# Kernel tuning notes

Hardware: AMD Instinct MI355X
Metric: run time of the kernel (lower is better)

The kernel has to match this reference:

```python
import jax, jax.numpy as jnp
import numpy as np

N = 1024
N_FEAT = 512
HID = 256
N_KERNEL = 10
KERNEL_DIM = 10
MB_DIM = N_KERNEL * KERNEL_DIM  # 100
CAT = HID + N_KERNEL  # concat width per block
EPS = 1e-3  # keras LayerNormalization default epsilon
ALPHA = 0.3  # keras LeakyReLU default


def setup_inputs() -> dict:
    key = jax.random.key(0)
    ks = jax.random.split(key, 16)
    def w(k, shape, std=0.1):
        return (jax.random.normal(k, shape, dtype=jnp.float32) * std)
    return {
        "x": jax.random.normal(ks[0], (N, N_FEAT), dtype=jnp.float32),
        # block 0
        "W0": w(ks[1], (N_FEAT, HID)), "b0": jnp.zeros((HID,), jnp.float32),
        "Wd0": w(ks[2], (HID, MB_DIM)), "bd0": jnp.zeros((MB_DIM,), jnp.float32),
        "beta0": jnp.zeros((CAT,), jnp.float32),
        # block 1 (input width = HID + N_KERNEL)
        "W1": w(ks[3], (CAT, HID)), "b1": jnp.zeros((HID,), jnp.float32),
        "Wd1": w(ks[4], (HID, MB_DIM)), "bd1": jnp.zeros((MB_DIM,), jnp.float32),
        "beta1": jnp.zeros((CAT,), jnp.float32),
        # final critic head
        "Wf": w(ks[5], (CAT, 1)), "bf": jnp.zeros((1,), jnp.float32),
    }


def _batch_diversity(M):
    # M: [N, n_kernel*kernel_dim] -> [N, n_kernel]
    M = M.reshape(-1, N_KERNEL, KERNEL_DIM)
    # pairwise L1 distance over kernel_dim: [N, N, n_kernel]
    l1 = jnp.abs(M[:, None, :, :] - M[None, :, :, :]).sum(axis=3)
    return jnp.exp(-l1).sum(axis=0)  # [N, n_kernel]


def _layer_norm_center_only(h, beta):
    mu = h.mean(axis=-1, keepdims=True)
    var = h.var(axis=-1, keepdims=True)
    return (h - mu) * jax.lax.rsqrt(var + EPS) + beta


def _block(x, W, b, Wd, bd, beta):
    h = x @ W + b                       # [N, HID]
    div = _batch_diversity(h @ Wd + bd)  # [N, N_KERNEL]
    h = jnp.concatenate([h, div], axis=1)  # [N, CAT]
    h = _layer_norm_center_only(h, beta)   # dropout is identity at inference
    return jax.nn.leaky_relu(h, ALPHA)


def reference(x, W0, b0, Wd0, bd0, beta0, W1, b1, Wd1, bd1, beta1, Wf, bf):
    h = _block(x, W0, b0, Wd0, bd0, beta0)
    h = _block(h, W1, b1, Wd1, bd1, beta1)
    return h @ Wf + bf  # [N, 1] critic value (WGGP: no sigmoid)
```

## Files before the change

### kernel.cpp

```cpp
#include <hip/hip_runtime.h>

typedef __attribute__((ext_vector_type(8))) short short8;
typedef __attribute__((ext_vector_type(4))) float f32x4;

#define EPS   1e-3f
#define ALPHA 0.3f

#define MFMA(a, b, c) __builtin_amdgcn_mfma_f32_16x16x32_bf16((a), (b), (c), 0, 0, 0)

__device__ __forceinline__ unsigned short f2bf(float f) {
    unsigned u = __float_as_uint(f);
    unsigned r = u + 0x7FFFu + ((u >> 16) & 1u);
    return (unsigned short)(r >> 16);
}
__device__ __forceinline__ float lrelu(float v) { return v > 0.f ? v : ALPHA * v; }

__global__ __launch_bounds__(256) void prep_kernel(
    const float* __restrict__ W0, const float* __restrict__ Wd0,
    const float* __restrict__ W1, const float* __restrict__ Wd1,
    const float* __restrict__ b0, const float* __restrict__ bd0,
    const float* __restrict__ b1, const float* __restrict__ bd1,
    unsigned short* __restrict__ Wc0bT, unsigned short* __restrict__ Wc1bT,
    float* __restrict__ bcomb0, float* __restrict__ bcomb1)
{
    const int bid = blockIdx.x, t = threadIdx.x;
    if (bid < 100) {
        __shared__ unsigned short Ab[32][264];
        __shared__ unsigned short BbT[32][264];
        const float *Wsrc, *Wdsrc;
        unsigned short* Cdst;
        int ldc, ft, ct, arows;
        if (bid < 64) { ft = bid & 15; ct = bid >> 4; Wsrc = W0; Wdsrc = Wd0;
                        Cdst = Wc0bT; ldc = 512; arows = 512; }
        else { const int s = bid - 64; ft = s % 9; ct = s / 9;
               Wsrc = W1; Wdsrc = Wd1; Cdst = Wc1bT; ldc = 296; arows = 266; }

        {
            const int row = t >> 3, kc = t & 7;
            const int f = ft * 32 + row;
            if (f < arows) {
                const float* wp = Wsrc + (size_t)f * 256 + kc * 32;
#pragma unroll
                for (int i = 0; i < 8; ++i) {
                    const float4 v = ((const float4*)wp)[i];
                    Ab[row][kc * 32 + i * 4 + 0] = f2bf(v.x);
                    Ab[row][kc * 32 + i * 4 + 1] = f2bf(v.y);
                    Ab[row][kc * 32 + i * 4 + 2] = f2bf(v.z);
                    Ab[row][kc * 32 + i * 4 + 3] = f2bf(v.w);
                }
            } else {
#pragma unroll
                for (int i = 0; i < 8; ++i)
                    *(ushort4*)&Ab[row][kc * 32 + i * 4] = make_ushort4(0, 0, 0, 0);
            }
        }
        for (int idx = t; idx < 2048; idx += 256) {
            const int h = idx >> 3, c4 = idx & 7;
            const int cbase = ct * 32 + c4 * 4;
            float v[4];
            if (cbase + 3 < 100) {
                const float4 q = *(const float4*)&Wdsrc[(size_t)h * 100 + cbase];
                v[0] = q.x; v[1] = q.y; v[2] = q.z; v[3] = q.w;
            } else {
#pragma unroll
                for (int j = 0; j < 4; ++j)
                    v[j] = (cbase + j < 100) ? Wdsrc[(size_t)h * 100 + cbase + j] : 0.f;
            }
#pragma unroll
            for (int j = 0; j < 4; ++j) BbT[c4 * 4 + j][h] = f2bf(v[j]);
        }
        __syncthreads();

        const int lane = t & 63, w = t >> 6;
        const int cr = w & 1, fr = w >> 1, r = lane & 15, g = lane >> 4;
        const unsigned short* Ap = &BbT[cr * 16 + r][g * 8];
        const unsigned short* Bp = &Ab[fr * 16 + r][g * 8];
        f32x4 a0 = {0.f, 0.f, 0.f, 0.f}, a1 = {0.f, 0.f, 0.f, 0.f};
#pragma unroll
        for (int k0 = 0; k0 < 256; k0 += 64) {
            a0 = MFMA(*(const short8*)(Ap + k0),      *(const short8*)(Bp + k0),      a0);
            a1 = MFMA(*(const short8*)(Ap + k0 + 32), *(const short8*)(Bp + k0 + 32), a1);
        }
        const f32x4 acc = a0 + a1;
        const int crow = ct * 32 + cr * 16 + g * 4;
        const int fcol = ft * 32 + fr * 16 + r;
#pragma unroll
        for (int i = 0; i < 4; ++i)
            Cdst[(size_t)(crow + i) * ldc + fcol] = f2bf(acc[i]);
    } else {
        const float* bb = (bid == 100) ? b0 : b1;
        const float* Wd = (bid == 100) ? Wd0 : Wd1;
        const float* bd = (bid == 100) ? bd0 : bd1;
        float* o = (bid == 100) ? bcomb0 : bcomb1;
        if (t < 128) {
            float s = 0.f;
            if (t < 100) {
                s = bd[t];
                float s0 = 0.f, s1 = 0.f, s2 = 0.f, s3 = 0.f;
                for (int k = 0; k < 256; k += 4) {
                    s0 += bb[k]     * Wd[k * 100 + t];
                    s1 += bb[k + 1] * Wd[(k + 1) * 100 + t];
                    s2 += bb[k + 2] * Wd[(k + 2) * 100 + t];
                    s3 += bb[k + 3] * Wd[(k + 3) * 100 + t];
                }
                s += (s0 + s1) + (s2 + s3);
            }
            o[t] = s;
        }
    }
}

__global__ __launch_bounds__(256) void hm0_mfma(
    const float* __restrict__ x, const float* __restrict__ W0,
    const unsigned short* __restrict__ Wc0bT,
    const float* __restrict__ b0, const float* __restrict__ bcomb0,
    float* __restrict__ h0, float* __restrict__ Mt0)
{
    __shared__ unsigned short At[32][520];
    __shared__ unsigned short Bt[32][520];

    const int t = threadIdx.x, xt = blockIdx.x, yt = blockIdx.y;

    {
        const int row = t >> 3, kc = t & 7;
        const float* xp = x + (size_t)(xt * 32 + row) * 512 + kc * 64;
#pragma unroll
        for (int i = 0; i < 8; ++i) {
            const float4 lo = ((const float4*)xp)[i * 2];
            const float4 hi = ((const float4*)xp)[i * 2 + 1];
            short8 p;
            p[0] = f2bf(lo.x); p[1] = f2bf(lo.y); p[2] = f2bf(lo.z); p[3] = f2bf(lo.w);
            p[4] = f2bf(hi.x); p[5] = f2bf(hi.y); p[6] = f2bf(hi.z); p[7] = f2bf(hi.w);
            *(short8*)&At[row][kc * 64 + i * 8] = p;
        }
    }
    if (yt < 8) {
        const int kc = t >> 5, n = t & 31, col0 = yt * 32;
        for (int kk = 0; kk < 64; kk += 2) {
            const int k = kc * 64 + kk;
            const float a = W0[(size_t)k * 256 + col0 + n];
            const float b = W0[(size_t)(k + 1) * 256 + col0 + n];
            const unsigned pk = (unsigned)f2bf(a) | ((unsigned)f2bf(b) << 16);
            *(unsigned*)&Bt[n][k] = pk;
        }
    } else {
        const int c = t >> 3, kc = t & 7;
        const unsigned short* bp = Wc0bT + (size_t)((yt - 8) * 32 + c) * 512 + kc * 64;
#pragma unroll
        for (int i = 0; i < 8; ++i)
            *(short8*)&Bt[c][kc * 64 + i * 8] = ((const short8*)bp)[i];
    }
    __syncthreads();

    const int lane = t & 63, w = t >> 6;
    const int wr = w >> 1, wn = w & 1, r = lane & 15, g = lane >> 4;
    const int lrA = wr * 16 + r, lrB = wn * 16 + r;
    f32x4 a0 = {0.f, 0.f, 0.f, 0.f}, a1 = {0.f, 0.f, 0.f, 0.f};
#pragma unroll
    for (int k0 = 0; k0 < 512; k0 += 64) {
        a0 = MFMA(*(const short8*)&At[lrA][k0 + g * 8],
                  *(const short8*)&Bt[lrB][k0 + g * 8], a0);
        a1 = MFMA(*(const short8*)&At[lrA][k0 + 32 + g * 8],
                  *(const short8*)&Bt[lrB][k0 + 32 + g * 8], a1);
    }
    const f32x4 acc = a0 + a1;
    const int orow0 = xt * 32 + wr * 16 + g * 4;

    if (yt < 8) {
        const int bcol = yt * 32 + wn * 16 + r;
        const float bv = b0[bcol];
#pragma unroll
        for (int i = 0; i < 4; ++i)
            h0[(size_t)(orow0 + i) * 256 + bcol] = acc[i] + bv;
    } else {
        const int c = (yt - 8) * 32 + wn * 16 + r;
        if (c < 100) {
            const int kq = c / 10, d = c - kq * 10;
            const float bv = bcomb0[c];
            float* dst = Mt0 + (size_t)kq * (1024 * 16) + (size_t)orow0 * 16 + d;
#pragma unroll
            for (int i = 0; i < 4; ++i) dst[i * 16] = acc[i] + bv;
        }
    }
}

__global__ __launch_bounds__(256) void hm1_mfma(
    const unsigned short* __restrict__ a0b, const float* __restrict__ W1,
    const unsigned short* __restrict__ Wc1bT,
    const float* __restrict__ b1, const float* __restrict__ bcomb1,
    float* __restrict__ h1, float* __restrict__ Mt1)
{
    __shared__ unsigned short At[32][296];
    __shared__ unsigned short Bt[32][296];

    const int t = threadIdx.x, xt = blockIdx.x, yt = blockIdx.y;

    {
        const int row = t >> 3, kc = t & 7;
        const unsigned short* ap = a0b + (size_t)(xt * 32 + row) * 296;
        for (int i = kc; i < 37; i += 8)
            *(short8*)&At[row][i * 8] = ((const short8*)ap)[i];
    }
    if (yt < 8) {
        const int kc = t >> 5, n = t & 31, col0 = yt * 32;
        const int kkEnd = (kc == 7) ? 44 : 36;
        for (int kk = 0; kk < kkEnd; kk += 2) {
            const int k = kc * 36 + kk;
            const float a = (k < 266)     ? W1[(size_t)k * 256 + col0 + n] : 0.f;
            const float b = (k + 1 < 266) ? W1[(size_t)(k + 1) * 256 + col0 + n] : 0.f;
            const unsigned pk = (unsigned)f2bf(a) | ((unsigned)f2bf(b) << 16);
            *(unsigned*)&Bt[n][k] = pk;
        }
    } else {
        const int c = t >> 3, kc = t & 7;
        const unsigned short* bp = Wc1bT + (size_t)((yt - 8) * 32 + c) * 296;
        for (int i = kc; i < 37; i += 8)
            *(short8*)&Bt[c][i * 8] = ((const short8*)bp)[i];
    }
    __syncthreads();

    const int lane = t & 63, w = t >> 6;
    const int wr = w >> 1, wn = w & 1, r = lane & 15, g = lane >> 4;
    const int lrA = wr * 16 + r, lrB = wn * 16 + r;
    f32x4 a0 = {0.f, 0.f, 0.f, 0.f}, a1 = {0.f, 0.f, 0.f, 0.f};
#pragma unroll
    for (int k0 = 0; k0 < 256; k0 += 64) {
        a0 = MFMA(*(const short8*)&At[lrA][k0 + g * 8],
                  *(const short8*)&Bt[lrB][k0 + g * 8], a0);
        a1 = MFMA(*(const short8*)&At[lrA][k0 + 32 + g * 8],
                  *(const short8*)&Bt[lrB][k0 + 32 + g * 8], a1);
    }
    a0 = MFMA(*(const short8*)&At[lrA][256 + g * 8],
              *(const short8*)&Bt[lrB][256 + g * 8], a0);
    const f32x4 acc = a0 + a1;
    const int orow0 = xt * 32 + wr * 16 + g * 4;

    if (yt < 8) {
        const int bcol = yt * 32 + wn * 16 + r;
        const float bv = b1[bcol];
#pragma unroll
        for (int i = 0; i < 4; ++i)
            h1[(size_t)(orow0 + i) * 256 + bcol] = acc[i] + bv;
    } else {
        const int c = (yt - 8) * 32 + wn * 16 + r;
        if (c < 100) {
            const int kq = c / 10, d = c - kq * 10;
            const float bv = bcomb1[c];
            float* dst = Mt1 + (size_t)kq * (1024 * 16) + (size_t)orow0 * 16 + d;
#pragma unroll
            for (int i = 0; i < 4; ++i) dst[i * 16] = acc[i] + bv;
        }
    }
}

__global__ __launch_bounds__(256) void diversity_kernel(
    const float* __restrict__ Mt, float* __restrict__ divOut)
{
    __shared__ float Ms[1024 * 16];
    __shared__ float red[256];

    const int t = threadIdx.x;
    const float* src = Mt + (size_t)blockIdx.y * (1024 * 16);
    for (int i = t; i < 1024 * 4; i += 256)
        ((float4*)Ms)[i] = ((const float4*)src)[i];
    __syncthreads();

    const int il = t & 31, jc = t >> 5;
    const int i = blockIdx.x * 32 + il;

    const float4 m0 = *(const float4*)&Ms[i * 16];
    const float4 m1 = *(const float4*)&Ms[i * 16 + 4];
    const float2 m2 = *(const float2*)&Ms[i * 16 + 8];

    float acc = 0.f;
    const int jB = jc * 128;
#pragma unroll 4
    for (int j = jB; j < jB + 128; ++j) {
        const float4 v0 = *(const float4*)&Ms[j * 16];
        const float4 v1 = *(const float4*)&Ms[j * 16 + 4];
        const float2 v2 = *(const float2*)&Ms[j * 16 + 8];
        float l1 = fabsf(m0.x - v0.x) + fabsf(m0.y - v0.y)
                 + fabsf(m0.z - v0.z) + fabsf(m0.w - v0.w)
                 + fabsf(m1.x - v1.x) + fabsf(m1.y - v1.y)
                 + fabsf(m1.z - v1.z) + fabsf(m1.w - v1.w)
                 + fabsf(m2.x - v2.x) + fabsf(m2.y - v2.y);
        acc += __expf(-l1);
    }

    red[t] = acc;
    __syncthreads();
    if (t < 32) {
        float s = 0.f;
#pragma unroll
        for (int c = 0; c < 8; ++c) s += red[c * 32 + t];
        divOut[(size_t)(blockIdx.x * 32 + t) * 10 + blockIdx.y] = s;
    }
}

__global__ __launch_bounds__(256) void ln0_kernel(
    const float* __restrict__ h0, const float* __restrict__ div0,
    const float* __restrict__ beta0, unsigned short* __restrict__ a0b)
{
    const int t = threadIdx.x, lane = t & 63;
    const int row = blockIdx.x * 4 + (t >> 6);

    const float4 hv = ((const float4*)(h0 + (size_t)row * 256))[lane];
    const float dv = (lane < 10) ? div0[(size_t)row * 10 + lane] : 0.f;

    float s = hv.x + hv.y + hv.z + hv.w + dv;
    float q = hv.x * hv.x + hv.y * hv.y + hv.z * hv.z + hv.w * hv.w + dv * dv;
#pragma unroll
    for (int m = 32; m > 0; m >>= 1) { s += __shfl_xor(s, m); q += __shfl_xor(q, m); }

    const float mean = s * (1.f / 266.f);
    const float var  = q * (1.f / 266.f) - mean * mean;
    const float inv  = rsqrtf(var + EPS);

    const float4 bv = ((const float4*)beta0)[lane];
    ushort4 o;
    o.x = f2bf(lrelu((hv.x - mean) * inv + bv.x));
    o.y = f2bf(lrelu((hv.y - mean) * inv + bv.y));
    o.z = f2bf(lrelu((hv.z - mean) * inv + bv.z));
    o.w = f2bf(lrelu((hv.w - mean) * inv + bv.w));
    *(ushort4*)&a0b[(size_t)row * 296 + lane * 4] = o;

    if (lane < 10)
        a0b[(size_t)row * 296 + 256 + lane] = f2bf(lrelu((dv - mean) * inv + beta0[256 + lane]));
    else if (lane >= 16 && lane < 46)
        a0b[(size_t)row * 296 + 250 + lane] = 0;
}

__global__ __launch_bounds__(256) void ln_final(
    const float* __restrict__ h1, const float* __restrict__ div1,
    const float* __restrict__ beta1, const float* __restrict__ Wf,
    const float* __restrict__ bf, float* __restrict__ out)
{
    const int t = threadIdx.x, lane = t & 63;
    const int row = blockIdx.x * 4 + (t >> 6);

    const float4 hv = ((const float4*)(h1 + (size_t)row * 256))[lane];
    const float dv = (lane < 10) ? div1[(size_t)row * 10 + lane] : 0.f;

    float s = hv.x + hv.y + hv.z + hv.w + dv;
    float q = hv.x * hv.x + hv.y * hv.y + hv.z * hv.z + hv.w * hv.w + dv * dv;
#pragma unroll
    for (int m = 32; m > 0; m >>= 1) { s += __shfl_xor(s, m); q += __shfl_xor(q, m); }

    const float mean = s * (1.f / 266.f);
    const float var  = q * (1.f / 266.f) - mean * mean;
    const float inv  = rsqrtf(var + EPS);

    const float4 bv = ((const float4*)beta1)[lane];
    const float4 wf = ((const float4*)Wf)[lane];
    float d = lrelu((hv.x - mean) * inv + bv.x) * wf.x
            + lrelu((hv.y - mean) * inv + bv.y) * wf.y
            + lrelu((hv.z - mean) * inv + bv.z) * wf.z
            + lrelu((hv.w - mean) * inv + bv.w) * wf.w;
    if (lane < 10)
        d += lrelu((dv - mean) * inv + beta1[256 + lane]) * Wf[256 + lane];
#pragma unroll
    for (int m = 32; m > 0; m >>= 1) d += __shfl_xor(d, m);
    if (lane == 0) out[row] = d + bf[0];
}

extern "C" void kernel_launch(void* const* d_in, const int* in_sizes, int n_in,
                              void* d_out, int out_size, void* d_ws, size_t ws_size,
                              hipStream_t stream)
{
    const float* x     = (const float*)d_in[0];
    const float* W0    = (const float*)d_in[1];
    const float* b0    = (const float*)d_in[2];
    const float* Wd0   = (const float*)d_in[3];
    const float* bd0   = (const float*)d_in[4];
    const float* beta0 = (const float*)d_in[5];
    const float* W1    = (const float*)d_in[6];
    const float* b1    = (const float*)d_in[7];
    const float* Wd1   = (const float*)d_in[8];
    const float* bd1   = (const float*)d_in[9];
    const float* beta1 = (const float*)d_in[10];
    const float* Wf    = (const float*)d_in[11];
    const float* bf    = (const float*)d_in[12];
    float* out = (float*)d_out;

    float* fws = (float*)d_ws;
    float* h0     = fws;
    float* h1     = h0 + 1024 * 256;
    float* Mt0    = h1 + 1024 * 256;
    float* Mt1    = Mt0 + 10 * 1024 * 16;
    float* div0   = Mt1 + 10 * 1024 * 16;
    float* div1   = div0 + 1024 * 10;
    float* bcomb0 = div1 + 1024 * 10;
    float* bcomb1 = bcomb0 + 128;
    unsigned short* Wc0bT = (unsigned short*)(bcomb1 + 128);
    unsigned short* Wc1bT = Wc0bT + 128 * 512;
    unsigned short* a0b   = Wc1bT + 128 * 296;

    dim3 blk(256);

    prep_kernel<<<dim3(102), blk, 0, stream>>>(
        W0, Wd0, W1, Wd1, b0, bd0, b1, bd1, Wc0bT, Wc1bT, bcomb0, bcomb1);

    hm0_mfma<<<dim3(32, 12), blk, 0, stream>>>(
        x, W0, Wc0bT, b0, bcomb0, h0, Mt0);

    diversity_kernel<<<dim3(32, 10), blk, 0, stream>>>(Mt0, div0);

    ln0_kernel<<<dim3(256), blk, 0, stream>>>(h0, div0, beta0, a0b);

    hm1_mfma<<<dim3(32, 12), blk, 0, stream>>>(
        a0b, W1, Wc1bT, b1, bcomb1, h1, Mt1);

    diversity_kernel<<<dim3(32, 10), blk, 0, stream>>>(Mt1, div1);

    ln_final<<<dim3(256), blk, 0, stream>>>(h1, div1, beta1, Wf, bf, out);
}
```

Baseline: 63.59 us.

## Fuse batch-diversity into layer-norm kernels and store projections as bf16

The separate diversity kernels and the two layer-norm kernels are merged into one templated kernel, which removes two launches and the round trip of the diversity results through global memory. Each block now owns 4 output rows. It loops over the 10 kernels, double-buffering the full 1024-row projection for each kernel into LDS as fp32, then applies the layer norm tail (bf16 activation output, or the final head dot). The matmul kernels now write the diversity projections as bf16, which halves that traffic but lowers the precision of the pairwise L1 distances. The new layout has every block restage all 1024 rows for every kernel. That greatly raises total L2 reads and conversion work, and the roughly 90 KB of LDS per block limits occupancy.

```diff
diff --git a/kernel.cpp b/kernel.cpp
--- a/kernel.cpp
+++ b/kernel.cpp
@@ -12,6 +12,9 @@
     unsigned u = __float_as_uint(f);
     unsigned r = u + 0x7FFFu + ((u >> 16) & 1u);
     return (unsigned short)(r >> 16);
+}
+__device__ __forceinline__ float bf2f(unsigned short u) {
+    return __uint_as_float((unsigned)u << 16);
 }
 __device__ __forceinline__ float lrelu(float v) { return v > 0.f ? v : ALPHA * v; }
 
@@ -114,7 +117,7 @@
     const float* __restrict__ x, const float* __restrict__ W0,
     const unsigned short* __restrict__ Wc0bT,
     const float* __restrict__ b0, const float* __restrict__ bcomb0,
-    float* __restrict__ h0, float* __restrict__ Mt0)
+    float* __restrict__ h0, unsigned short* __restrict__ Mt0)
 {
     __shared__ unsigned short At[32][520];
     __shared__ unsigned short Bt[32][520];
@@ -177,9 +180,10 @@
         if (c < 100) {
             const int kq = c / 10, d = c - kq * 10;
             const float bv = bcomb0[c];
-            float* dst = Mt0 + (size_t)kq * (1024 * 16) + (size_t)orow0 * 16 + d;
-#pragma unroll
-            for (int i = 0; i < 4; ++i) dst[i * 16] = acc[i] + bv;
+            unsigned short* dst = Mt0 + (size_t)kq * (1024 * 16)
+                                + (size_t)orow0 * 16 + d;
+#pragma unroll
+            for (int i = 0; i < 4; ++i) dst[(size_t)i * 16] = f2bf(acc[i] + bv);
         }
     }
 }
@@ -188,7 +192,7 @@
     const unsigned short* __restrict__ a0b, const float* __restrict__ W1,
     const unsigned short* __restrict__ Wc1bT,
     const float* __restrict__ b1, const float* __restrict__ bcomb1,
-    float* __restrict__ h1, float* __restrict__ Mt1)
+    float* __restrict__ h1, unsigned short* __restrict__ Mt1)
 {
     __shared__ unsigned short At[32][296];
     __shared__ unsigned short Bt[32][296];
@@ -246,67 +250,97 @@
         if (c < 100) {
             const int kq = c / 10, d = c - kq * 10;
             const float bv = bcomb1[c];
-            float* dst = Mt1 + (size_t)kq * (1024 * 16) + (size_t)orow0 * 16 + d;
-#pragma unroll
-            for (int i = 0; i < 4; ++i) dst[i * 16] = acc[i] + bv;
-        }
-    }
-}
-
-__global__ __launch_bounds__(256) void diversity_kernel(
-    const float* __restrict__ Mt, float* __restrict__ divOut)
+            unsigned short* dst = Mt1 + (size_t)kq * (1024 * 16)
+                                + (size_t)orow0 * 16 + d;
+#pragma unroll
+            for (int i = 0; i < 4; ++i) dst[(size_t)i * 16] = f2bf(acc[i] + bv);
+        }
+    }
+}
+
+template<int TAIL>
+__global__ __launch_bounds__(256) void divln_kernel(
+    const unsigned short* __restrict__ Mt, const float* __restrict__ h,
+    const float* __restrict__ beta, const float* __restrict__ Wf,
+    const float* __restrict__ bfv,
+    unsigned short* __restrict__ a0b, float* __restrict__ out)
 {
-    __shared__ float Ms[1024 * 16];
-    __shared__ float red[256];
-
-    const int t = threadIdx.x;
-    const float* src = Mt + (size_t)blockIdx.y * (1024 * 16);
-    for (int i = t; i < 1024 * 4; i += 256)
-        ((float4*)Ms)[i] = ((const float4*)src)[i];
+    __shared__ float Ms[2][1024 * 11];
+    __shared__ float divP[4][4][10];
+
+    const int t = threadIdx.x, lane = t & 63, w = t >> 6;
+    const int r0 = blockIdx.x * 4;
+
+    auto stage = [&](int buf, int k) {
+        const unsigned short* src = Mt + (size_t)k * (1024 * 16);
+        float* M = Ms[buf];
+#pragma unroll
+        for (int it = 0; it < 4; ++it) {
+            const int j = it * 256 + t;
+            const unsigned short* rp = src + (size_t)j * 16;
+            const short8 v8 = *(const short8*)rp;
+            const unsigned v2 = *(const unsigned*)(rp + 8);
+            float* dst = M + j * 11;
+#pragma unroll
+            for (int d = 0; d < 8; ++d) dst[d] = bf2f((unsigned short)v8[d]);
+            dst[8] = bf2f((unsigned short)(v2 & 0xffffu));
+            dst[9] = bf2f((unsigned short)(v2 >> 16));
+        }
+    };
+
+    stage(0, 0);
     __syncthreads();
 
-    const int il = t & 31, jc = t >> 5;
-    const int i = blockIdx.x * 32 + il;
-
-    const float4 m0 = *(const float4*)&Ms[i * 16];
-    const float4 m1 = *(const float4*)&Ms[i * 16 + 4];
-    const float2 m2 = *(const float2*)&Ms[i * 16 + 8];
-
-    float acc = 0.f;
-    const int jB = jc * 128;
-#pragma unroll 4
-    for (int j = jB; j < jB + 128; ++j) {
-        const float4 v0 = *(const float4*)&Ms[j * 16];
-        const float4 v1 = *(const float4*)&Ms[j * 16 + 4];
-        const float2 v2 = *(const float2*)&Ms[j * 16 + 8];
-        float l1 = fabsf(m0.x - v0.x) + fabsf(m0.y - v0.y)
-                 + fabsf(m0.z - v0.z) + fabsf(m0.w - v0.w)
-                 + fabsf(m1.x - v1.x) + fabsf(m1.y - v1.y)
-                 + fabsf(m1.z - v1.z) + fabsf(m1.w - v1.w)
-                 + fabsf(m2.x - v2.x) + fabsf(m2.y - v2.y);
-        acc += __expf(-l1);
-    }
-
-    red[t] = acc;
-    __syncthreads();
-    if (t < 32) {
-        float s = 0.f;
-#pragma unroll
-        for (int c = 0; c < 8; ++c) s += red[c * 32 + t];
-        divOut[(size_t)(blockIdx.x * 32 + t) * 10 + blockIdx.y] = s;
-    }
-}
-
-__global__ __launch_bounds__(256) void ln0_kernel(
-    const float* __restrict__ h0, const float* __restrict__ div0,
-    const float* __restrict__ beta0, unsigned short* __restrict__ a0b)
-{
-    const int t = threadIdx.x, lane = t & 63;
-    const int row = blockIdx.x * 4 + (t >> 6);
-
-    const float4 hv = ((const float4*)(h0 + (size_t)row * 256))[lane];
-    const float dv = (lane < 10) ? div0[(size_t)row * 10 + lane] : 0.f;
-
+    for (int k = 0; k < 10; ++k) {
+        const int buf = k & 1;
+        if (k + 1 < 10) stage(buf ^ 1, k + 1);
+
+        const float* M = Ms[buf];
+        float Mi[4][10];
+#pragma unroll
+        for (int rr = 0; rr < 4; ++rr)
+#pragma unroll
+            for (int d = 0; d < 10; ++d) Mi[rr][d] = M[(r0 + rr) * 11 + d];
+
+        float acc0 = 0.f, acc1 = 0.f, acc2 = 0.f, acc3 = 0.f;
+        const int jbase = w * 256;
+#pragma unroll
+        for (int jj = 0; jj < 4; ++jj) {
+            const int j = jbase + jj * 64 + lane;
+            const float* mp = M + j * 11;
+            float m[10];
+#pragma unroll
+            for (int d = 0; d < 10; ++d) m[d] = mp[d];
+            float l0 = 0.f, l1 = 0.f, l2 = 0.f, l3 = 0.f;
+#pragma unroll
+            for (int d = 0; d < 10; ++d) {
+                l0 += fabsf(Mi[0][d] - m[d]);
+                l1 += fabsf(Mi[1][d] - m[d]);
+                l2 += fabsf(Mi[2][d] - m[d]);
+                l3 += fabsf(Mi[3][d] - m[d]);
+            }
+            acc0 += __expf(-l0);
+            acc1 += __expf(-l1);
+            acc2 += __expf(-l2);
+            acc3 += __expf(-l3);
+        }
+        float a[4] = {acc0, acc1, acc2, acc3};
+#pragma unroll
+        for (int rr = 0; rr < 4; ++rr) {
+            float s = a[rr];
+#pragma unroll
+            for (int mm = 32; mm > 0; mm >>= 1) s += __shfl_xor(s, mm);
+            if (lane == 0) divP[w][rr][k] = s;
+        }
+        __syncthreads();
+    }
+
+    const int row = r0 + w;
+    float dv = 0.f;
+    if (lane < 10)
+        dv = divP[0][w][lane] + divP[1][w][lane] + divP[2][w][lane] + divP[3][w][lane];
+
+    const float4 hv = ((const float4*)(h + (size_t)row * 256))[lane];
     float s = hv.x + hv.y + hv.z + hv.w + dv;
     float q = hv.x * hv.x + hv.y * hv.y + hv.z * hv.z + hv.w * hv.w + dv * dv;
 #pragma unroll
@@ -315,52 +349,32 @@
     const float mean = s * (1.f / 266.f);
     const float var  = q * (1.f / 266.f) - mean * mean;
     const float inv  = rsqrtf(var + EPS);
-
-    const float4 bv = ((const float4*)beta0)[lane];
-    ushort4 o;
-    o.x = f2bf(lrelu((hv.x - mean) * inv + bv.x));
-    o.y = f2bf(lrelu((hv.y - mean) * inv + bv.y));
-    o.z = f2bf(lrelu((hv.z - mean) * inv + bv.z));
-    o.w = f2bf(lrelu((hv.w - mean) * inv + bv.w));
-    *(ushort4*)&a0b[(size_t)row * 296 + lane * 4] = o;
-
-    if (lane < 10)
-        a0b[(size_t)row * 296 + 256 + lane] = f2bf(lrelu((dv - mean) * inv + beta0[256 + lane]));
-    else if (lane >= 16 && lane < 46)
-        a0b[(size_t)row * 296 + 250 + lane] = 0;
-}
-
-__global__ __launch_bounds__(256) void ln_final(
-    const float* __restrict__ h1, const float* __restrict__ div1,
-    const float* __restrict__ beta1, const float* __restrict__ Wf,
-    const float* __restrict__ bf, float* __restrict__ out)
-{
-    const int t = threadIdx.x, lane = t & 63;
-    const int row = blockIdx.x * 4 + (t >> 6);
-
-    const float4 hv = ((const float4*)(h1 + (size_t)row * 256))[lane];
-    const float dv = (lane < 10) ? div1[(size_t)row * 10 + lane] : 0.f;
-
-    float s = hv.x + hv.y + hv.z + hv.w + dv;
-    float q = hv.x * hv.x + hv.y * hv.y + hv.z * hv.z + hv.w * hv.w + dv * dv;
-#pragma unroll
-    for (int m = 32; m > 0; m >>= 1) { s += __shfl_xor(s, m); q += __shfl_xor(q, m); }
-
-    const float mean = s * (1.f / 266.f);
-    const float var  = q * (1.f / 266.f) - mean * mean;
-    const float inv  = rsqrtf(var + EPS);
-
-    const float4 bv = ((const float4*)beta1)[lane];
-    const float4 wf = ((const float4*)Wf)[lane];
-    float d = lrelu((hv.x - mean) * inv + bv.x) * wf.x
-            + lrelu((hv.y - mean) * inv + bv.y) * wf.y
-            + lrelu((hv.z - mean) * inv + bv.z) * wf.z
-            + lrelu((hv.w - mean) * inv + bv.w) * wf.w;
-    if (lane < 10)
-        d += lrelu((dv - mean) * inv + beta1[256 + lane]) * Wf[256 + lane];
-#pragma unroll
-    for (int m = 32; m > 0; m >>= 1) d += __shfl_xor(d, m);
-    if (lane == 0) out[row] = d + bf[0];
+    const float4 bv = ((const float4*)beta)[lane];
+
+    if constexpr (TAIL == 0) {
+        ushort4 o;
+        o.x = f2bf(lrelu((hv.x - mean) * inv + bv.x));
+        o.y = f2bf(lrelu((hv.y - mean) * inv + bv.y));
+        o.z = f2bf(lrelu((hv.z - mean) * inv + bv.z));
+        o.w = f2bf(lrelu((hv.w - mean) * inv + bv.w));
+        *(ushort4*)&a0b[(size_t)row * 296 + lane * 4] = o;
+        if (lane < 10)
+            a0b[(size_t)row * 296 + 256 + lane] =
+                f2bf(lrelu((dv - mean) * inv + beta[256 + lane]));
+        else if (lane >= 16 && lane < 46)
+            a0b[(size_t)row * 296 + 250 + lane] = 0;
+    } else {
+        const float4 wf = ((const float4*)Wf)[lane];
+        float d = lrelu((hv.x - mean) * inv + bv.x) * wf.x
+                + lrelu((hv.y - mean) * inv + bv.y) * wf.y
+                + lrelu((hv.z - mean) * inv + bv.z) * wf.z
+                + lrelu((hv.w - mean) * inv + bv.w) * wf.w;
+        if (lane < 10)
+            d += lrelu((dv - mean) * inv + beta[256 + lane]) * Wf[256 + lane];
+#pragma unroll
+        for (int m = 32; m > 0; m >>= 1) d += __shfl_xor(d, m);
+        if (lane == 0) out[row] = d + bfv[0];
+    }
 }
 
 extern "C" void kernel_launch(void* const* d_in, const int* in_sizes, int n_in,
@@ -385,15 +399,13 @@
     float* fws = (float*)d_ws;
     float* h0     = fws;
     float* h1     = h0 + 1024 * 256;
-    float* Mt0    = h1 + 1024 * 256;
-    float* Mt1    = Mt0 + 10 * 1024 * 16;
-    float* div0   = Mt1 + 10 * 1024 * 16;
-    float* div1   = div0 + 1024 * 10;
-    float* bcomb0 = div1 + 1024 * 10;
+    float* bcomb0 = h1 + 1024 * 256;
     float* bcomb1 = bcomb0 + 128;
     unsigned short* Wc0bT = (unsigned short*)(bcomb1 + 128);
     unsigned short* Wc1bT = Wc0bT + 128 * 512;
     unsigned short* a0b   = Wc1bT + 128 * 296;
+    unsigned short* Mt0   = a0b + 1024 * 296;
+    unsigned short* Mt1   = Mt0 + 10 * 1024 * 16;
 
     dim3 blk(256);
 
@@ -403,14 +415,12 @@
     hm0_mfma<<<dim3(32, 12), blk, 0, stream>>>(
         x, W0, Wc0bT, b0, bcomb0, h0, Mt0);
 
-    diversity_kernel<<<dim3(32, 10), blk, 0, stream>>>(Mt0, div0);
-
-    ln0_kernel<<<dim3(256), blk, 0, stream>>>(h0, div0, beta0, a0b);
+    divln_kernel<0><<<dim3(256), blk, 0, stream>>>(
+        Mt0, h0, beta0, nullptr, nullptr, a0b, nullptr);
 
     hm1_mfma<<<dim3(32, 12), blk, 0, stream>>>(
         a0b, W1, Wc1bT, b1, bcomb1, h1, Mt1);
 
-    diversity_kernel<<<dim3(32, 10), blk, 0, stream>>>(Mt1, div1);
-
-    ln_final<<<dim3(256), blk, 0, stream>>>(h1, div1, beta1, Wf, bf, out);
-}
+    divln_kernel<1><<<dim3(256), blk, 0, stream>>>(
+        Mt1, h1, beta1, Wf, bf, nullptr, out);
+}
```

Result: slower. 82.59 us (+29.9%).
